# Performance work log

Measured on AMD Instinct MI355X. Metric: run time of the kernel, lower is better.

## Reference

```python
import jax, jax.numpy as jnp
import numpy as np

DIM = 1024
ATT_DIM = 1024
NUM_HEADS = 16
HEAD_DIM = ATT_DIM // NUM_HEADS


def setup_inputs() -> dict:
    key = jax.random.key(0)
    ks = jax.random.split(key, 13)
    s = lambda fan_in: 1.0 / np.sqrt(fan_in)
    bsz, n = 8, 1024
    x = jax.random.normal(ks[0], (bsz, n, DIM), dtype=jnp.float32)
    # Linear weights stored as [in, out] (apply via x @ W + b)
    Wq = jax.random.uniform(ks[1], (DIM, ATT_DIM), minval=-s(DIM), maxval=s(DIM))
    bq = jax.random.uniform(ks[2], (ATT_DIM,), minval=-s(DIM), maxval=s(DIM))
    Wk = jax.random.uniform(ks[3], (DIM, ATT_DIM), minval=-s(DIM), maxval=s(DIM))
    bk = jax.random.uniform(ks[4], (ATT_DIM,), minval=-s(DIM), maxval=s(DIM))
    Wv = jax.random.uniform(ks[5], (DIM, ATT_DIM), minval=-s(DIM), maxval=s(DIM))
    bv = jax.random.uniform(ks[6], (ATT_DIM,), minval=-s(DIM), maxval=s(DIM))
    Win = jax.random.uniform(ks[7], (DIM, HEAD_DIM), minval=-s(DIM), maxval=s(DIM))
    bin_ = jax.random.uniform(ks[8], (HEAD_DIM,), minval=-s(DIM), maxval=s(DIM))
    d_in1 = HEAD_DIM * (NUM_HEADS + 1)
    W1 = jax.random.uniform(ks[9], (d_in1, 2 * DIM), minval=-s(d_in1), maxval=s(d_in1))
    b1 = jax.random.uniform(ks[10], (2 * DIM,), minval=-s(d_in1), maxval=s(d_in1))
    W2 = jax.random.uniform(ks[11], (2 * DIM, DIM), minval=-s(2 * DIM), maxval=s(2 * DIM))
    b2 = jax.random.uniform(ks[12], (DIM,), minval=-s(2 * DIM), maxval=s(2 * DIM))
    return {"x": x, "Wq": Wq, "bq": bq, "Wk": Wk, "bk": bk, "Wv": Wv, "bv": bv,
            "Win": Win, "bin_": bin_, "W1": W1, "b1": b1, "W2": W2, "b2": b2}


def reference(x, Wq, bq, Wk, bk, Wv, bv, Win, bin_, W1, b1, W2, b2):
    bsz, n, _ = x.shape
    scaling = HEAD_DIM ** (-0.5)
    # [b, n, h, d]
    q = (x @ Wq + bq).reshape(bsz, n, NUM_HEADS, HEAD_DIM) * scaling
    k = (x @ Wk + bk).reshape(bsz, n, NUM_HEADS, HEAD_DIM)
    v = (x @ Wv + bv).reshape(bsz, n, NUM_HEADS, HEAD_DIM)
    # scores [b, h, n, n]
    score = jnp.einsum('bihd,bjhd->bhij', q, k)
    diag = jnp.eye(n, dtype=bool)  # self positions masked with -inf
    score = jnp.where(diag[None, None], -jnp.inf, score)
    attn = jax.nn.softmax(score, axis=-1)
    out = jnp.einsum('bhij,bjhd->bihd', attn, v).reshape(bsz, n, NUM_HEADS * HEAD_DIM)
    in_ = (x @ Win + bin_)  # [b, n, head_dim]
    out = jnp.concatenate([out, in_], axis=-1)
    h = jax.nn.relu(out @ W1 + b1)
    return h @ W2 + b2
```

## Files before the change

### kernel.cpp

```cpp
#include <hip/hip_runtime.h>

typedef __bf16 bf16;
typedef __attribute__((ext_vector_type(8))) __bf16 bf16x8;
typedef __attribute__((ext_vector_type(4))) __bf16 bf16x4;
typedef __attribute__((ext_vector_type(4))) short short4_t;
typedef __attribute__((ext_vector_type(4))) float floatx4;

typedef const void __attribute__((address_space(1)))* gas1p;
typedef void __attribute__((address_space(3)))* las3p;

#define LOG2E 1.44269504088896340736f

static constexpr int D_MODEL = 1024;
static constexpr int N_HEADS = 16;
static constexpr int HDIM    = 64;
static constexpr int BSZ     = 8;
static constexpr int SEQ     = 1024;
static constexpr int ROWS    = BSZ * SEQ;
static constexpr int FF_IN   = 1088;
static constexpr int FF_HID  = 2048;
static constexpr int QKV_LD  = 3072;

__device__ __forceinline__ floatx4 mfma_bf16(bf16x8 a, bf16x8 b, floatx4 c) {
  return __builtin_amdgcn_mfma_f32_16x16x32_bf16(a, b, c, 0, 0, 0);
}

__device__ __forceinline__ floatx4 mfma16(bf16x4 a, bf16x4 b, floatx4 c) {
#if __has_builtin(__builtin_amdgcn_mfma_f32_16x16x16_bf16)
  return __builtin_amdgcn_mfma_f32_16x16x16_bf16(a, b, c, 0, 0, 0);
#else
  return __builtin_amdgcn_mfma_f32_16x16x16bf16_1k(
      __builtin_bit_cast(short4_t, a), __builtin_bit_cast(short4_t, b), c, 0, 0, 0);
#endif
}

__device__ __forceinline__ float fast_exp2(float x) {
#if __has_builtin(__builtin_amdgcn_exp2f)
  return __builtin_amdgcn_exp2f(x);
#else
  return exp2f(x);
#endif
}

__device__ __forceinline__ float flex_load(const void* src, size_t idx, int isbf) {
  return isbf ? (float)((const bf16*)src)[idx] : ((const float*)src)[idx];
}

__global__ void detect_kernel(const unsigned* __restrict__ w, int* __restrict__ flag) {
  __shared__ int cnt;
  if (threadIdx.x == 0) cnt = 0;
  __syncthreads();
  int hits = 0;
  for (int i = threadIdx.x; i < 4096; i += 256) {
    const unsigned v = w[(size_t)i * 997 + 13];
    const unsigned b = (v >> 8) & 0x7F;
    hits += (b >= 0x3B && b <= 0x41) ? 1 : 0;
  }
  atomicAdd(&cnt, hits);
  __syncthreads();
  if (threadIdx.x == 0) *flag = (cnt > 2048) ? 1 : 0;
}

struct TransJobs {
  const void* src[6];
  bf16* dst[6];
  int R[6], C[6];
  int tiles_x[6];
  int tile_base[7];
  float scale[6];
};

static constexpr int NBX = (ROWS * D_MODEL) / 2048;
static constexpr int NBB = 25;

__global__ __launch_bounds__(256)
void prep_all_kernel(const void* __restrict__ xsrc, bf16* __restrict__ xdst,
                     const void* bq, const void* bk, const void* bv,
                     const void* bin, const void* b1, const void* b2,
                     float* __restrict__ biasf, TransJobs J,
                     const int* __restrict__ flag) {
  __shared__ float tile[32][33];
  const int isbf = *flag;
  const int bid = blockIdx.x;

  if (bid < NBX) {
    const size_t i = ((size_t)bid * 256 + threadIdx.x) * 8;
    bf16x8 o;
    if (isbf) {
      o = *reinterpret_cast<const bf16x8*>((const bf16*)xsrc + i);
    } else {
      const float4 f0 = *reinterpret_cast<const float4*>((const float*)xsrc + i);
      const float4 f1 = *reinterpret_cast<const float4*>((const float*)xsrc + i + 4);
      o[0] = (bf16)f0.x; o[1] = (bf16)f0.y; o[2] = (bf16)f0.z; o[3] = (bf16)f0.w;
      o[4] = (bf16)f1.x; o[5] = (bf16)f1.y; o[6] = (bf16)f1.z; o[7] = (bf16)f1.w;
    }
    *reinterpret_cast<bf16x8*>(xdst + i) = o;
    return;
  }
  if (bid < NBX + NBB) {
    const int i = (bid - NBX) * 256 + threadIdx.x;
    if (i < 1024)      biasf[i] = flex_load(bq, i, isbf) * (0.125f * LOG2E);
    else if (i < 2048) biasf[i] = flex_load(bk, i - 1024, isbf);
    else if (i < 3072) biasf[i] = flex_load(bv, i - 2048, isbf);
    else if (i < 3136) biasf[i] = flex_load(bin, i - 3072, isbf);
    else if (i < 5184) biasf[i] = flex_load(b1, i - 3136, isbf);
    else if (i < 6208) biasf[i] = flex_load(b2, i - 5184, isbf);
    return;
  }
  const int tb = bid - (NBX + NBB);
  int j = 0;
#pragma unroll
  for (int t = 1; t < 6; t++) j += (tb >= J.tile_base[t]) ? 1 : 0;
  const int t = tb - J.tile_base[j];
  const int c0 = (t % J.tiles_x[j]) * 32, r0 = (t / J.tiles_x[j]) * 32;
  const void* src = J.src[j];
  bf16* dst = J.dst[j];
  const int R = J.R[j], C = J.C[j];
  const float scale = J.scale[j];
  const int tx = threadIdx.x & 31, ty = threadIdx.x >> 5;
  for (int i = ty; i < 32; i += 8)
    tile[i][tx] = flex_load(src, (size_t)(r0 + i) * C + (c0 + tx), isbf);
  __syncthreads();
  for (int i = ty; i < 32; i += 8)
    dst[(size_t)(c0 + i) * R + (r0 + tx)] = (bf16)(tile[tx][i] * scale);
}

template <int BN, bool DO_RELU, bool OUT_FLEX, bool V_TRANS>
__global__ __launch_bounds__(256)
void gemm_bt(const bf16* __restrict__ A, const bf16* __restrict__ BT,
             const float* __restrict__ bias,
             void* __restrict__ Cv, int N, int K, int ldc,
             bf16* __restrict__ C2, int ldc2, int nsplit, int nvalid,
             int gy, bf16* __restrict__ vt_out,
             const int* __restrict__ flag) {
  constexpr int BM = 128, BK = 64;
  constexpr int TCN = BN / 32;
  constexpr int ACH = (BM * BK) / (256 * 8);
  constexpr int BCH = (BN * BK) / (256 * 8);
  __shared__ __align__(16) char smem_raw[(BM * BK + BN * BK) * 2];
  bf16* As = (bf16*)smem_raw;
  bf16* Bs = As + BM * BK;
  const int tid = threadIdx.x;
  const int wave = tid >> 6, lane = tid & 63;
  const int quad = lane >> 4, lo = lane & 15;
  const int wm = wave >> 1, wn = wave & 1;

  int m0, n0;
  if (gy == 0) {
    m0 = blockIdx.x * BM;
    n0 = blockIdx.y * BN;
  } else {
    const int nwg = gridDim.x;
    const int bid = blockIdx.x;
    const int sid = (bid & 7) * (nwg >> 3) + (bid >> 3);
    const int P = gy << 3;
    const int g = sid / P, r2 = sid - g * P;
    m0 = (g * 8 + (r2 & 7)) * BM;
    n0 = (r2 >> 3) * BN;
  }

  floatx4 acc[4][TCN];
#pragma unroll
  for (int i = 0; i < 4; i++)
#pragma unroll
    for (int j = 0; j < TCN; j++) acc[i][j] = floatx4{0.f, 0.f, 0.f, 0.f};

  for (int kb = 0; kb < K; kb += BK) {
#pragma unroll
    for (int u = 0; u < ACH; u++) {
      const int c = u * 256 + tid;
      const int row = c >> 3, col = c & 7;
      const int gcol = col ^ (row & 7);
      const bf16* gp = A + (size_t)(m0 + row) * K + kb + gcol * 8;
      __builtin_amdgcn_global_load_lds((gas1p)gp, (las3p)(As + c * 8), 16, 0, 0);
    }
#pragma unroll
    for (int u = 0; u < BCH; u++) {
      const int c = u * 256 + tid;
      const int row = c >> 3, col = c & 7;
      const int gcol = col ^ (row & 7);
      const bf16* gp = BT + (size_t)(n0 + row) * K + kb + gcol * 8;
      __builtin_amdgcn_global_load_lds((gas1p)gp, (las3p)(Bs + c * 8), 16, 0, 0);
    }
    __syncthreads();
#pragma unroll
    for (int kk = 0; kk < 2; kk++) {
      bf16x8 af[4], bfr[TCN];
#pragma unroll
      for (int tr = 0; tr < 4; tr++) {
        const int row = wm * 64 + tr * 16 + lo;
        const int cc = (kk * 4 + quad) ^ (lo & 7);
        af[tr] = *reinterpret_cast<const bf16x8*>(As + row * BK + cc * 8);
      }
#pragma unroll
      for (int tc = 0; tc < TCN; tc++) {
        const int row = wn * (BN / 2) + tc * 16 + lo;
        const int cc = (kk * 4 + quad) ^ (lo & 7);
        bfr[tc] = *reinterpret_cast<const bf16x8*>(Bs + row * BK + cc * 8);
      }
#pragma unroll
      for (int tr = 0; tr < 4; tr++)
#pragma unroll
        for (int tc = 0; tc < TCN; tc++)
          acc[tr][tc] = mfma_bf16(af[tr], bfr[tc], acc[tr][tc]);
    }
    __syncthreads();
  }

  if (V_TRANS && n0 >= 2048 && n0 < 3072) {
    const int h = ((n0 - 2048) >> 6) + wn;
    const int b = m0 >> 10;
    const int ibase = (m0 & 1023) + wm * 64;
    bf16* L = ((bf16*)smem_raw) + wave * 4096;
#pragma unroll
    for (int tc = 0; tc < TCN; tc++) {
      const int d = tc * 16 + lo;
      const float bval = bias[n0 + wn * 64 + d];
#pragma unroll
      for (int tr = 0; tr < 4; tr++) {
        const int iin = tr * 16 + quad * 4;
        bf16x4 p;
#pragma unroll
        for (int rr = 0; rr < 4; rr++) p[rr] = (bf16)(acc[tr][tc][rr] + bval);
        *reinterpret_cast<bf16x4*>(L + d * 64 + (iin ^ ((d & 7) << 3))) = p;
      }
    }
    asm volatile("s_waitcnt lgkmcnt(0)" ::: "memory");
    bf16* dst = vt_out + (size_t)(b * 16 + h) * (HDIM * SEQ) + ibase;
#pragma unroll
    for (int w8 = 0; w8 < 8; w8++) {
      const int dp = w8 * 8 + (lane >> 3);
      const int ip = (lane & 7) * 8;
      const bf16x8 v = *reinterpret_cast<const bf16x8*>(
          L + dp * 64 + (ip ^ ((dp & 7) << 3)));
      *reinterpret_cast<bf16x8*>(dst + (size_t)dp * SEQ + ip) = v;
    }
    return;
  }

  const int isbf = OUT_FLEX ? *flag : 1;
#pragma unroll
  for (int tc = 0; tc < TCN; tc++) {
    const int col = n0 + wn * (BN / 2) + tc * 16 + lo;
    const float bval = bias[col];
    if (col < nsplit) {
#pragma unroll
      for (int tr = 0; tr < 4; tr++) {
        const int rbase = m0 + wm * 64 + tr * 16 + quad * 4;
#pragma unroll
        for (int rr = 0; rr < 4; rr++) {
          float v = acc[tr][tc][rr] + bval;
          if (DO_RELU) v = fmaxf(v, 0.f);
          const size_t idx = (size_t)(rbase + rr) * ldc + col;
          if (!OUT_FLEX || isbf) ((bf16*)Cv)[idx] = (bf16)v;
          else                   ((float*)Cv)[idx] = v;
        }
      }
    } else if (col < nvalid) {
#pragma unroll
      for (int tr = 0; tr < 4; tr++) {
        const int rbase = m0 + wm * 64 + tr * 16 + quad * 4;
#pragma unroll
        for (int rr = 0; rr < 4; rr++) {
          float v = acc[tr][tc][rr] + bval;
          if (DO_RELU) v = fmaxf(v, 0.f);
          C2[(size_t)(rbase + rr) * ldc2 + (col - nsplit)] = (bf16)v;
        }
      }
    }
  }
}

__global__ __launch_bounds__(256)
void attn_kernel(const bf16* __restrict__ QKV, const bf16* __restrict__ Vt,
                 bf16* __restrict__ Cc) {
  __shared__ bf16 Ks[64 * 64];
  __shared__ bf16 Vs[64 * 64];
  const int bid = blockIdx.x;
  const int xcd = bid & 7, g = bid >> 3;
  const int ib = g & 15, bh = (g >> 4) * 8 + xcd;
  const int b = bh >> 4, h = bh & 15;
  const int i0 = ib * 64;
  const int tid = threadIdx.x, wave = tid >> 6, lane = tid & 63;
  const int quad = lane >> 4, lo = lane & 15;
  const int iw = i0 + wave * 16;
  const bf16* qptr = QKV + (size_t)b * SEQ * QKV_LD + h * HDIM;
  const bf16* kptr = QKV + (size_t)b * SEQ * QKV_LD + 1024 + h * HDIM;
  const bf16* vptr = Vt + (size_t)bh * HDIM * SEQ;

  bf16x8 qf[2];
#pragma unroll
  for (int kf = 0; kf < 2; kf++)
    qf[kf] = *reinterpret_cast<const bf16x8*>(
        qptr + (size_t)(iw + lo) * QKV_LD + kf * 32 + quad * 8);

  floatx4 oacc[4];
  float lrow = 0.f;
#pragma unroll
  for (int dt = 0; dt < 4; dt++) oacc[dt] = floatx4{0.f, 0.f, 0.f, 0.f};

  for (int jb = 0; jb < SEQ / 64; jb++) {
    const int j0 = jb * 64;
#pragma unroll
    for (int u = 0; u < 2; u++) {
      const int c = u * 256 + tid;
      const int row = c >> 3, col = c & 7;
      const int gcol = col ^ (row & 7);
      __builtin_amdgcn_global_load_lds(
          (gas1p)(kptr + (size_t)(j0 + row) * QKV_LD + gcol * 8),
          (las3p)(Ks + c * 8), 16, 0, 0);
      __builtin_amdgcn_global_load_lds(
          (gas1p)(vptr + (size_t)row * SEQ + j0 + gcol * 8),
          (las3p)(Vs + c * 8), 16, 0, 0);
    }
    __syncthreads();

    floatx4 sacc[4];
#pragma unroll
    for (int mt = 0; mt < 4; mt++) sacc[mt] = floatx4{0.f, 0.f, 0.f, 0.f};
    __builtin_amdgcn_s_setprio(1);
#pragma unroll
    for (int mt = 0; mt < 4; mt++) {
      const int r = mt * 16 + lo;
      const int cc0 = quad ^ (lo & 7);
      const int cc1 = (4 + quad) ^ (lo & 7);
      const bf16x8 k0 = *reinterpret_cast<const bf16x8*>(Ks + r * 64 + cc0 * 8);
      const bf16x8 k1 = *reinterpret_cast<const bf16x8*>(Ks + r * 64 + cc1 * 8);
      sacc[mt] = mfma_bf16(k0, qf[0], sacc[mt]);
      sacc[mt] = mfma_bf16(k1, qf[1], sacc[mt]);
    }
    __builtin_amdgcn_s_setprio(0);

    if (j0 == i0) {
      const int ig = iw + lo;
#pragma unroll
      for (int mt = 0; mt < 4; mt++)
#pragma unroll
        for (int r = 0; r < 4; r++)
          if (j0 + mt * 16 + quad * 4 + r == ig) sacc[mt][r] = -1e30f;
    }

    bf16x4 pfrag[4];
    {
      float s0 = 0.f, s1 = 0.f;
#pragma unroll
      for (int mt = 0; mt < 4; mt++) {
        bf16x4 pk;
#pragma unroll
        for (int r = 0; r < 4; r++) {
          const float p = fast_exp2(sacc[mt][r]);
          if (mt & 1) s1 += p; else s0 += p;
          pk[r] = (bf16)p;
        }
        pfrag[mt] = pk;
      }
      float s = s0 + s1;
      s += __shfl_xor(s, 16);
      s += __shfl_xor(s, 32);
      lrow += s;
    }

    __builtin_amdgcn_s_setprio(1);
#pragma unroll
    for (int dt = 0; dt < 4; dt++) {
      const int r = dt * 16 + lo;
#pragma unroll
      for (int kt = 0; kt < 4; kt++) {
        const int gch = kt * 2 + (quad >> 1);
        const int cc = gch ^ (lo & 7);
        const bf16x4 vf = *reinterpret_cast<const bf16x4*>(
            Vs + r * 64 + cc * 8 + (quad & 1) * 4);
        oacc[dt] = mfma16(vf, pfrag[kt], oacc[dt]);
      }
    }
    __builtin_amdgcn_s_setprio(0);
    __syncthreads();
  }

  {
    const int ig = iw + lo;
    const float inv = 1.0f / lrow;
    bf16* cb = Cc + ((size_t)b * SEQ + ig) * FF_IN + h * HDIM;
#pragma unroll
    for (int dt = 0; dt < 4; dt++) {
      bf16x4 o;
#pragma unroll
      for (int r = 0; r < 4; r++) o[r] = (bf16)(oacc[dt][r] * inv);
      *reinterpret_cast<bf16x4*>(cb + dt * 16 + quad * 4) = o;
    }
  }
}

extern "C" void kernel_launch(void* const* d_in, const int* in_sizes, int n_in,
                              void* d_out, int out_size, void* d_ws, size_t ws_size,
                              hipStream_t stream) {
  (void)in_sizes; (void)n_in; (void)out_size; (void)ws_size;
  const void* x   = d_in[0];
  const void* Wq  = d_in[1];
  const void* bq  = d_in[2];
  const void* Wk  = d_in[3];
  const void* bk  = d_in[4];
  const void* Wv  = d_in[5];
  const void* bv  = d_in[6];
  const void* Win = d_in[7];
  const void* bin = d_in[8];
  const void* W1  = d_in[9];
  const void* b1  = d_in[10];
  const void* W2  = d_in[11];
  const void* b2  = d_in[12];

  size_t off = 0;
  char* wsb = (char*)d_ws;
  auto alloc = [&](size_t bytes) {
    void* p = (void*)(wsb + off);
    off += (bytes + 255) & ~(size_t)255;
    return p;
  };
  int*   flag  = (int*)alloc(4);
  bf16*  xbf   = (bf16*)alloc((size_t)ROWS * D_MODEL * 2);
  bf16*  WqkvT = (bf16*)alloc((size_t)3200 * 1024 * 2);
  bf16*  W1T   = (bf16*)alloc((size_t)FF_HID * FF_IN * 2);
  bf16*  W2T   = (bf16*)alloc((size_t)D_MODEL * FF_HID * 2);
  float* biasf = (float*)alloc(6208 * 4);
  bf16*  qkv   = (bf16*)alloc((size_t)ROWS * QKV_LD * 2);
  bf16*  vtb   = (bf16*)alloc((size_t)ROWS * D_MODEL * 2);
  bf16*  cbuf  = (bf16*)alloc((size_t)ROWS * FF_IN * 2);
  bf16*  hbuf  = (bf16*)alloc((size_t)ROWS * FF_HID * 2);
  float* b1f   = biasf + 3136;
  float* b2f   = biasf + 5184;

  const dim3 blk(256);
  detect_kernel<<<1, blk, 0, stream>>>((const unsigned*)x, flag);

  TransJobs J;
  J.src[0] = Wq;  J.dst[0] = WqkvT;                        J.R[0] = 1024; J.C[0] = 1024; J.scale[0] = 0.125f * LOG2E;
  J.src[1] = Wk;  J.dst[1] = WqkvT + (size_t)1024 * 1024;  J.R[1] = 1024; J.C[1] = 1024; J.scale[1] = 1.0f;
  J.src[2] = Wv;  J.dst[2] = WqkvT + (size_t)2048 * 1024;  J.R[2] = 1024; J.C[2] = 1024; J.scale[2] = 1.0f;
  J.src[3] = Win; J.dst[3] = WqkvT + (size_t)3072 * 1024;  J.R[3] = 1024; J.C[3] = 64;   J.scale[3] = 1.0f;
  J.src[4] = W1;  J.dst[4] = W1T;                          J.R[4] = 1088; J.C[4] = 2048; J.scale[4] = 1.0f;
  J.src[5] = W2;  J.dst[5] = W2T;                          J.R[5] = 2048; J.C[5] = 1024; J.scale[5] = 1.0f;
  int base = 0;
  for (int j = 0; j < 6; j++) {
    J.tiles_x[j] = J.C[j] / 32;
    J.tile_base[j] = base;
    base += (J.R[j] / 32) * (J.C[j] / 32);
  }
  J.tile_base[6] = base;

  prep_all_kernel<<<dim3(NBX + NBB + base), blk, 0, stream>>>(
      x, xbf, bq, bk, bv, bin, b1, b2, biasf, J, flag);

  gemm_bt<128, false, false, true><<<dim3(1600), blk, 0, stream>>>(
      xbf, WqkvT, biasf, qkv, 3200, 1024, QKV_LD,
      cbuf + 1024, FF_IN, 3072, 3136, 25, vtb, nullptr);

  attn_kernel<<<dim3(2048), blk, 0, stream>>>(qkv, vtb, cbuf);

  gemm_bt<128, true, false, false><<<dim3(64, 16), blk, 0, stream>>>(
      cbuf, W1T, b1f, hbuf, FF_HID, FF_IN, FF_HID,
      nullptr, 0, FF_HID, FF_HID, 0, nullptr, nullptr);
  gemm_bt<128, false, true, false><<<dim3(64, 8), blk, 0, stream>>>(
      hbuf, W2T, b2f, d_out, D_MODEL, FF_HID, D_MODEL,
      nullptr, 0, D_MODEL, D_MODEL, 0, nullptr, flag);
}
```

Baseline: 381.0 us.

## Fold dtype detection into prep kernel and register-prefetch K/V tiles in attention

```diff
diff --git a/kernel.cpp b/kernel.cpp
--- a/kernel.cpp
+++ b/kernel.cpp
@@ -46,21 +46,6 @@
   return isbf ? (float)((const bf16*)src)[idx] : ((const float*)src)[idx];
 }
 
-__global__ void detect_kernel(const unsigned* __restrict__ w, int* __restrict__ flag) {
-  __shared__ int cnt;
-  if (threadIdx.x == 0) cnt = 0;
-  __syncthreads();
-  int hits = 0;
-  for (int i = threadIdx.x; i < 4096; i += 256) {
-    const unsigned v = w[(size_t)i * 997 + 13];
-    const unsigned b = (v >> 8) & 0x7F;
-    hits += (b >= 0x3B && b <= 0x41) ? 1 : 0;
-  }
-  atomicAdd(&cnt, hits);
-  __syncthreads();
-  if (threadIdx.x == 0) *flag = (cnt > 2048) ? 1 : 0;
-}
-
 struct TransJobs {
   const void* src[6];
   bf16* dst[6];
@@ -78,10 +63,20 @@
                      const void* bq, const void* bk, const void* bv,
                      const void* bin, const void* b1, const void* b2,
                      float* __restrict__ biasf, TransJobs J,
-                     const int* __restrict__ flag) {
+                     int* __restrict__ flagOut) {
   __shared__ float tile[32][33];
-  const int isbf = *flag;
+  __shared__ int cnt;
+  if (threadIdx.x == 0) cnt = 0;
+  __syncthreads();
+  {
+    const unsigned v = ((const unsigned*)xsrc)[(size_t)threadIdx.x * 997 + 13];
+    const unsigned bb = (v >> 8) & 0x7F;
+    if (bb >= 0x3B && bb <= 0x41) atomicAdd(&cnt, 1);
+  }
+  __syncthreads();
+  const int isbf = (cnt > 128) ? 1 : 0;
   const int bid = blockIdx.x;
+  if (bid == NBX && threadIdx.x == 0) *flagOut = isbf;
 
   if (bid < NBX) {
     const size_t i = ((size_t)bid * 256 + threadIdx.x) * 8;
@@ -288,6 +283,10 @@
   const bf16* kptr = QKV + (size_t)b * SEQ * QKV_LD + 1024 + h * HDIM;
   const bf16* vptr = Vt + (size_t)bh * HDIM * SEQ;
 
+  const int c0 = tid, c1 = 256 + tid;
+  const int row0 = c0 >> 3, gcol0 = (c0 & 7) ^ (row0 & 7);
+  const int row1 = c1 >> 3, gcol1 = (c1 & 7) ^ (row1 & 7);
+
   bf16x8 qf[2];
 #pragma unroll
   for (int kf = 0; kf < 2; kf++)
@@ -299,21 +298,34 @@
 #pragma unroll
   for (int dt = 0; dt < 4; dt++) oacc[dt] = floatx4{0.f, 0.f, 0.f, 0.f};
 
+  bf16x8 kreg0 = *reinterpret_cast<const bf16x8*>(
+      kptr + (size_t)row0 * QKV_LD + gcol0 * 8);
+  bf16x8 kreg1 = *reinterpret_cast<const bf16x8*>(
+      kptr + (size_t)row1 * QKV_LD + gcol1 * 8);
+  bf16x8 vreg0 = *reinterpret_cast<const bf16x8*>(
+      vptr + (size_t)row0 * SEQ + gcol0 * 8);
+  bf16x8 vreg1 = *reinterpret_cast<const bf16x8*>(
+      vptr + (size_t)row1 * SEQ + gcol1 * 8);
+
   for (int jb = 0; jb < SEQ / 64; jb++) {
     const int j0 = jb * 64;
-#pragma unroll
-    for (int u = 0; u < 2; u++) {
-      const int c = u * 256 + tid;
-      const int row = c >> 3, col = c & 7;
-      const int gcol = col ^ (row & 7);
-      __builtin_amdgcn_global_load_lds(
-          (gas1p)(kptr + (size_t)(j0 + row) * QKV_LD + gcol * 8),
-          (las3p)(Ks + c * 8), 16, 0, 0);
-      __builtin_amdgcn_global_load_lds(
-          (gas1p)(vptr + (size_t)row * SEQ + j0 + gcol * 8),
-          (las3p)(Vs + c * 8), 16, 0, 0);
-    }
     __syncthreads();
+    *reinterpret_cast<bf16x8*>(Ks + c0 * 8) = kreg0;
+    *reinterpret_cast<bf16x8*>(Ks + c1 * 8) = kreg1;
+    *reinterpret_cast<bf16x8*>(Vs + c0 * 8) = vreg0;
+    *reinterpret_cast<bf16x8*>(Vs + c1 * 8) = vreg1;
+    __syncthreads();
+    if (jb + 1 < SEQ / 64) {
+      const int jn = j0 + 64;
+      kreg0 = *reinterpret_cast<const bf16x8*>(
+          kptr + (size_t)(jn + row0) * QKV_LD + gcol0 * 8);
+      kreg1 = *reinterpret_cast<const bf16x8*>(
+          kptr + (size_t)(jn + row1) * QKV_LD + gcol1 * 8);
+      vreg0 = *reinterpret_cast<const bf16x8*>(
+          vptr + (size_t)row0 * SEQ + jn + gcol0 * 8);
+      vreg1 = *reinterpret_cast<const bf16x8*>(
+          vptr + (size_t)row1 * SEQ + jn + gcol1 * 8);
+    }
 
     floatx4 sacc[4];
 #pragma unroll
@@ -374,7 +386,6 @@
       }
     }
     __builtin_amdgcn_s_setprio(0);
-    __syncthreads();
   }
 
   {
@@ -430,7 +441,6 @@
   float* b2f   = biasf + 5184;
 
   const dim3 blk(256);
-  detect_kernel<<<1, blk, 0, stream>>>((const unsigned*)x, flag);
 
   TransJobs J;
   J.src[0] = Wq;  J.dst[0] = WqkvT;                        J.R[0] = 1024; J.C[0] = 1024; J.scale[0] = 0.125f * LOG2E;
```

Measured after the change: 380.1 us. Within noise of the previous version (-0.2%).
